# Kernel optimization log

Hardware: AMD Instinct MI355X
Metric: run time of the kernel (lower is better)

## Reference

```python
import jax, jax.numpy as jnp
import numpy as np

EPS = 1e-8  # RMSNormMultiHead default eps (forward passes self.eps)


def rms_norm_multihead(x, weight):
    # x: (B, L, H, d); normalize over last dim in float32, then scale per (H, d)
    x32 = x.astype(jnp.float32)
    normed = x32 * jax.lax.rsqrt(jnp.mean(x32 * x32, axis=-1, keepdims=True) + EPS)
    return normed.astype(x.dtype) * weight


def setup_inputs() -> dict:
    key = jax.random.key(0)
    k0, k1, k2 = jax.random.split(key, 3)
    B, L, D, H = 2, 1024, 1024, 16
    d = D // H
    X = jax.random.normal(k0, (B, L, D), dtype=jnp.float32)
    Wq = jax.random.normal(k1, (D, D), dtype=jnp.float32) * 0.02  # q_proj weight (out, in)
    Wv = jax.random.normal(k2, (D, D), dtype=jnp.float32) * 0.02  # v_proj weight (out, in)
    q_norm_w = jnp.ones((H, d), dtype=jnp.float32)
    v_norm_w = jnp.ones((H, d), dtype=jnp.float32)
    return {"X": X, "Wq": Wq, "Wv": Wv, "q_norm_w": q_norm_w, "v_norm_w": v_norm_w}


def reference(X, Wq, Wv, q_norm_w, v_norm_w):
    B, L, D = X.shape
    H, d = q_norm_w.shape
    K = X.reshape(B, L, H, d)
    Q = rms_norm_multihead((X @ Wq.T).reshape(B, L, H, d), q_norm_w)
    V = rms_norm_multihead((X @ Wv.T).reshape(B, L, H, d), v_norm_w)
    # cumulative outer-product KV state: (B, L, H, d, e)
    W = jnp.cumsum(jnp.einsum('blhd,blhe->blhde', K, V), axis=1)
    out = jnp.einsum('blhd,blhde->blhe', Q, W).reshape(B, L, D)
    return out
```

## Files before the change

kernel.cpp:

```cpp
#include <hip/hip_runtime.h>

#define BB 2
#define LL 1024
#define DD 1024
#define HH 16
#define NC 16
#define EPSF 1e-8f

typedef __attribute__((ext_vector_type(8))) short bf16x8;
typedef __attribute__((ext_vector_type(4))) float f32x4;
typedef unsigned short u16;

static __device__ inline u16 f2bf(float f) {
    unsigned int u = __builtin_bit_cast(unsigned int, f);
    u += 0x7fff + ((u >> 16) & 1);
    return (u16)(u >> 16);
}
static __device__ inline float bf2f(u16 v) {
    unsigned int u = ((unsigned int)v) << 16;
    return __builtin_bit_cast(float, u);
}
static __device__ inline void gload_lds16(const u16* g, u16* l) {
    __builtin_amdgcn_global_load_lds((const __attribute__((address_space(1))) void*)g,
                                     (__attribute__((address_space(3))) void*)l, 16, 0, 0);
}

__global__ __launch_bounds__(256) void cvt_k(const float* __restrict__ X,
                                             const float* __restrict__ Wq,
                                             const float* __restrict__ Wv,
                                             u16* __restrict__ Xb,
                                             u16* __restrict__ Wqb,
                                             u16* __restrict__ Wvb)
{
    int i = (blockIdx.x * 256 + threadIdx.x) * 4;
    const float* s; u16* d; int off;
    if (i < 2*1024*1024)      { s = X;  d = Xb;  off = i; }
    else if (i < 3*1024*1024) { s = Wq; d = Wqb; off = i - 2*1024*1024; }
    else                      { s = Wv; d = Wvb; off = i - 3*1024*1024; }
    float4 v = *(const float4*)(s + off);
    ushort4 o;
    o.x = f2bf(v.x); o.y = f2bf(v.y); o.z = f2bf(v.z); o.w = f2bf(v.w);
    *(ushort4*)(d + off) = o;
}

__global__ __launch_bounds__(256) void gemm_fused(const u16* __restrict__ Xb,
                                                  const u16* __restrict__ Wqb,
                                                  const u16* __restrict__ Wvb,
                                                  const float* __restrict__ qw,
                                                  const float* __restrict__ vw,
                                                  u16* __restrict__ Qb,
                                                  u16* __restrict__ Vb,
                                                  u16* __restrict__ S)
{
    const int K = DD, N = DD;
    const u16* W = blockIdx.z ? Wvb : Wqb;
    const float* nw = blockIdx.z ? vw : qw;
    u16* Y = blockIdx.z ? Vb : Qb;

    __shared__ alignas(16) char smem[49152];
    u16* Ab = (u16*)smem;
    u16* Bb = (u16*)(smem + 32768);

    const int tid = threadIdx.x, w = tid >> 6, lane = tid & 63;
    const int quad = lane >> 4, l16 = lane & 15;
    const int m0 = blockIdx.y * 128, n0 = blockIdx.x * 64;

    const int lr8 = lane >> 3;
    const int lc8 = (lane & 7) ^ lr8;
    const u16* gA = Xb + (size_t)(m0 + w*32 + lr8) * K + lc8 * 8;
    const u16* gB = W  + (size_t)(n0 + w*16 + lr8) * K + lc8 * 8;

    f32x4 acc[2][4] = {};

    auto stage = [&](int buf, int k0) {
        u16* As = Ab + buf * (128*64);
        u16* Bs = Bb + buf * (64*64);
        #pragma unroll
        for (int q = 0; q < 4; ++q)
            gload_lds16(gA + k0 + (size_t)q*8*K, As + (w*32 + q*8)*64);
        #pragma unroll
        for (int q = 0; q < 2; ++q)
            gload_lds16(gB + k0 + (size_t)q*8*K, Bs + (w*16 + q*8)*64);
    };
    auto compute = [&](int buf) {
        const u16* As = Ab + buf * (128*64);
        const u16* Bs = Bb + buf * (64*64);
        #pragma unroll
        for (int hh = 0; hh < 2; ++hh) {
            const int co = (((hh << 2) | quad) ^ (l16 & 7)) * 8;
            bf16x8 af[2], bfr[4];
            #pragma unroll
            for (int i = 0; i < 2; ++i)
                af[i] = *(const bf16x8*)&As[(w*32 + i*16 + l16) * 64 + co];
            #pragma unroll
            for (int j = 0; j < 4; ++j)
                bfr[j] = *(const bf16x8*)&Bs[(j*16 + l16) * 64 + co];
            #pragma unroll
            for (int i = 0; i < 2; ++i)
                #pragma unroll
                for (int j = 0; j < 4; ++j)
                    acc[i][j] = __builtin_amdgcn_mfma_f32_16x16x32_bf16(af[i], bfr[j], acc[i][j], 0, 0, 0);
        }
    };

    stage(0, 0);
    __syncthreads();
    int cur = 0;
    for (int k0 = 0; k0 < K; k0 += 64) {
        if (k0 + 64 < K) stage(cur ^ 1, k0 + 64);
        compute(cur);
        __syncthreads();
        cur ^= 1;
    }

    u16 (*Vt)[136] = (u16 (*)[136])smem;
    u16 (*Kt)[136] = (u16 (*)[136])(smem + 17408);

    float wv4[4];
    #pragma unroll
    for (int j = 0; j < 4; ++j) wv4[j] = nw[n0 + j*16 + l16];
    #pragma unroll
    for (int i = 0; i < 2; ++i) {
        float ss[4];
        #pragma unroll
        for (int r = 0; r < 4; ++r) {
            float s = 0.f;
            #pragma unroll
            for (int j = 0; j < 4; ++j) s += acc[i][j][r] * acc[i][j][r];
            ss[r] = s;
        }
        #pragma unroll
        for (int off = 1; off < 16; off <<= 1)
            #pragma unroll
            for (int r = 0; r < 4; ++r) ss[r] += __shfl_xor(ss[r], off, 64);
        float sc[4];
        #pragma unroll
        for (int r = 0; r < 4; ++r) sc[r] = rsqrtf(ss[r] * (1.f/64.f) + EPSF);
        #pragma unroll
        for (int r = 0; r < 4; ++r) {
            u16* yp = Y + (size_t)(m0 + w*32 + i*16 + quad*4 + r) * N + n0;
            #pragma unroll
            for (int j = 0; j < 4; ++j) {
                u16 val = f2bf(acc[i][j][r] * sc[r] * wv4[j]);
                yp[j*16 + l16] = val;
                if (blockIdx.z)
                    Vt[j*16 + l16][w*32 + i*16 + quad*4 + r] = val;
            }
        }
    }

    if (blockIdx.z) {
        {
            const int row = tid >> 1, q2 = tid & 1;
            size_t gb = (size_t)(m0 + row) * DD + n0 + q2 * 32;
            u16 kk[32];
            #pragma unroll
            for (int i2 = 0; i2 < 32; i2 += 4)
                *(ushort4*)&kk[i2] = *(const ushort4*)(Xb + gb + i2);
            #pragma unroll
            for (int i2 = 0; i2 < 32; ++i2)
                Kt[q2*32 + i2][row] = kk[i2];
        }
        __syncthreads();
        const int me = (w & 1) * 32, nd = (w >> 1) * 32;
        const int b = m0 >> 10, c0 = (m0 & 1023) >> 6, h = blockIdx.x;
        const int bh = b * HH + h;
        #pragma unroll
        for (int cc = 0; cc < 2; ++cc) {
            f32x4 sacc[2][2] = {};
            #pragma unroll
            for (int k0 = 0; k0 < 64; k0 += 32) {
                bf16x8 av[2], bv[2];
                #pragma unroll
                for (int i2 = 0; i2 < 2; ++i2)
                    av[i2] = *(const bf16x8*)&Vt[me + i2*16 + l16][cc*64 + k0 + quad*8];
                #pragma unroll
                for (int j2 = 0; j2 < 2; ++j2)
                    bv[j2] = *(const bf16x8*)&Kt[nd + j2*16 + l16][cc*64 + k0 + quad*8];
                #pragma unroll
                for (int i2 = 0; i2 < 2; ++i2)
                    #pragma unroll
                    for (int j2 = 0; j2 < 2; ++j2)
                        sacc[i2][j2] = __builtin_amdgcn_mfma_f32_16x16x32_bf16(av[i2], bv[j2], sacc[i2][j2], 0, 0, 0);
            }
            u16* Sp = S + ((size_t)((bh << 4) | (c0 + cc)) << 12) + w*1024;
            #pragma unroll
            for (int i2 = 0; i2 < 2; ++i2)
                #pragma unroll
                for (int j2 = 0; j2 < 2; ++j2)
                    #pragma unroll
                    for (int r = 0; r < 4; ++r)
                        Sp[(i2*2 + j2)*256 + r*64 + lane] = f2bf(sacc[i2][j2][r]);
        }
    }
}

__global__ __launch_bounds__(256) void out_k2(const u16* __restrict__ Xb,
                                              const u16* __restrict__ Qb,
                                              const u16* __restrict__ Vb,
                                              const u16* __restrict__ S,
                                              float* __restrict__ out)
{
    const int c = 15 - (blockIdx.x & 15);
    const int bh = blockIdx.x >> 4;
    const int h = bh & 15, b = bh >> 4;
    __shared__ u16 Qs[64][72];
    __shared__ u16 Ks[64][72];
    __shared__ u16 Vt[64][72];
    __shared__ u16 St[64][72];
    const int tid = threadIdx.x;
    {
        const int row = tid >> 2, q = tid & 3;
        size_t gbase = (size_t)(b*LL + c*64 + row) * DD + h*64 + q*16;
        u16 vv[16];
        #pragma unroll
        for (int i = 0; i < 16; i += 4) {
            *(ushort4*)&Qs[row][q*16 + i] = *(const ushort4*)(Qb + gbase + i);
            *(ushort4*)&Ks[row][q*16 + i] = *(const ushort4*)(Xb + gbase + i);
            *(ushort4*)&vv[i] = *(const ushort4*)(Vb + gbase + i);
        }
        #pragma unroll
        for (int i = 0; i < 16; ++i)
            Vt[q*16 + i][row] = vv[i];
        float facc[16] = {};
        const u16* Sbase = S + ((size_t)(bh * NC) << 12);
        int cp = 0;
        for (; cp + 4 <= c; cp += 4) {
            ushort4 sv[4][4];
            #pragma unroll
            for (int u = 0; u < 4; ++u)
                #pragma unroll
                for (int jj = 0; jj < 4; ++jj)
                    sv[u][jj] = *(const ushort4*)(Sbase + ((size_t)(cp + u) << 12) + tid*4 + jj*1024);
            #pragma unroll
            for (int u = 0; u < 4; ++u)
                #pragma unroll
                for (int jj = 0; jj < 4; ++jj) {
                    facc[jj*4+0] += bf2f(sv[u][jj].x);
                    facc[jj*4+1] += bf2f(sv[u][jj].y);
                    facc[jj*4+2] += bf2f(sv[u][jj].z);
                    facc[jj*4+3] += bf2f(sv[u][jj].w);
                }
        }
        for (; cp < c; ++cp) {
            const u16* Sc = Sbase + ((size_t)cp << 12);
            #pragma unroll
            for (int jj = 0; jj < 4; ++jj) {
                ushort4 sv = *(const ushort4*)(Sc + tid*4 + jj*1024);
                facc[jj*4+0] += bf2f(sv.x);
                facc[jj*4+1] += bf2f(sv.y);
                facc[jj*4+2] += bf2f(sv.z);
                facc[jj*4+3] += bf2f(sv.w);
            }
        }
        #pragma unroll
        for (int jj = 0; jj < 4; ++jj) {
            int g = tid * 4;
            int ij = (g >> 8) & 3, r = (g >> 6) & 3, ln = g & 63;
            int e = (jj & 1)*32 + (ij >> 1)*16 + (ln >> 4)*4 + r;
            int d = (jj >> 1)*32 + (ij & 1)*16 + (ln & 15);
            ushort4 o;
            o.x = f2bf(facc[jj*4+0]);
            o.y = f2bf(facc[jj*4+1]);
            o.z = f2bf(facc[jj*4+2]);
            o.w = f2bf(facc[jj*4+3]);
            *(ushort4*)&St[e][d] = o;
        }
    }
    __syncthreads();
    const int w = tid >> 6, lane = tid & 63, quad = lane >> 4, l16 = lane & 15;
    const int mo = (w & 1) * 32, no = (w >> 1) * 32;

    f32x4 pacc[2][2] = {};
    #pragma unroll
    for (int k0 = 0; k0 < 64; k0 += 32) {
        bf16x8 aq[2], bk[2];
        #pragma unroll
        for (int i = 0; i < 2; ++i)
            aq[i] = *(const bf16x8*)&Qs[mo + i*16 + l16][k0 + quad*8];
        #pragma unroll
        for (int j = 0; j < 2; ++j)
            bk[j] = *(const bf16x8*)&Ks[no + j*16 + l16][k0 + quad*8];
        #pragma unroll
        for (int i = 0; i < 2; ++i)
            #pragma unroll
            for (int j = 0; j < 2; ++j)
                pacc[i][j] = __builtin_amdgcn_mfma_f32_16x16x32_bf16(aq[i], bk[j], pacc[i][j], 0, 0, 0);
    }
    __syncthreads();
    #pragma unroll
    for (int i = 0; i < 2; ++i)
        #pragma unroll
        for (int j = 0; j < 2; ++j)
            #pragma unroll
            for (int r = 0; r < 4; ++r) {
                int l  = mo + i*16 + quad*4 + r;
                int lp = no + j*16 + l16;
                Ks[l][lp] = (lp <= l) ? f2bf(pacc[i][j][r]) : (u16)0;
            }
    __syncthreads();

    f32x4 acc[2][2] = {};
    #pragma unroll
    for (int k0 = 0; k0 < 64; k0 += 32) {
        bf16x8 a1[2], b1[2], a2[2], b2[2];
        #pragma unroll
        for (int i = 0; i < 2; ++i) {
            a1[i] = *(const bf16x8*)&Ks[mo + i*16 + l16][k0 + quad*8];
            a2[i] = *(const bf16x8*)&Qs[mo + i*16 + l16][k0 + quad*8];
        }
        #pragma unroll
        for (int j = 0; j < 2; ++j) {
            b1[j] = *(const bf16x8*)&Vt[no + j*16 + l16][k0 + quad*8];
            b2[j] = *(const bf16x8*)&St[no + j*16 + l16][k0 + quad*8];
        }
        #pragma unroll
        for (int i = 0; i < 2; ++i)
            #pragma unroll
            for (int j = 0; j < 2; ++j) {
                acc[i][j] = __builtin_amdgcn_mfma_f32_16x16x32_bf16(a1[i], b1[j], acc[i][j], 0, 0, 0);
                acc[i][j] = __builtin_amdgcn_mfma_f32_16x16x32_bf16(a2[i], b2[j], acc[i][j], 0, 0, 0);
            }
    }
    float* op = out + (size_t)(b*LL + c*64) * DD + h*64;
    #pragma unroll
    for (int i = 0; i < 2; ++i)
        #pragma unroll
        for (int j = 0; j < 2; ++j)
            #pragma unroll
            for (int r = 0; r < 4; ++r)
                op[(size_t)(mo + i*16 + quad*4 + r) * DD + no + j*16 + l16] = acc[i][j][r];
}

extern "C" void kernel_launch(void* const* d_in, const int* in_sizes, int n_in,
                              void* d_out, int out_size, void* d_ws, size_t ws_size,
                              hipStream_t stream) {
    const float* X  = (const float*)d_in[0];
    const float* Wq = (const float*)d_in[1];
    const float* Wv = (const float*)d_in[2];
    const float* qw = (const float*)d_in[3];
    const float* vw = (const float*)d_in[4];
    float* out = (float*)d_out;

    u16* Xb  = (u16*)d_ws;
    u16* Wqb = Xb  + (size_t)2*1024*1024;
    u16* Wvb = Wqb + (size_t)1024*1024;
    u16* Qb  = Wvb + (size_t)1024*1024;
    u16* Vb  = Qb  + (size_t)2*1024*1024;
    u16* S   = Vb  + (size_t)2*1024*1024;

    cvt_k<<<4096, 256, 0, stream>>>(X, Wq, Wv, Xb, Wqb, Wvb);
    gemm_fused<<<dim3(16, 16, 2), 256, 0, stream>>>(Xb, Wqb, Wvb, qw, vw, Qb, Vb, S);
    out_k2<<<BB*HH*NC, 256, 0, stream>>>(Xb, Qb, Vb, S, out);
}
```

Before: 96.96 us.

## Merge three kernels into one cooperative kernel with grid-wide syncs

Replaces the convert, GEMM+norm+chunk-state, and output kernels with a single persistent cooperative kernel of 512 blocks that uses grid syncs between phases. The aim is to remove the launch overhead and inter-kernel gaps of three separate dispatches. In exchange, every phase is fixed at 512 blocks, so the convert phase loops 8 times per thread. Grid barriers add their own latency, and the launch bound of 2 blocks per CU may constrain registers.

Measured after the change: 331.6 us. +242.0%, slower.

```diff
diff --git a/kernel.cpp b/kernel.cpp
--- a/kernel.cpp
+++ b/kernel.cpp
@@ -1,4 +1,6 @@
 #include <hip/hip_runtime.h>
+#include <hip/hip_cooperative_groups.h>
+namespace cg = cooperative_groups;
 
 #define BB 2
 #define LL 1024
@@ -25,311 +27,310 @@
                                      (__attribute__((address_space(3))) void*)l, 16, 0, 0);
 }
 
-__global__ __launch_bounds__(256) void cvt_k(const float* __restrict__ X,
-                                             const float* __restrict__ Wq,
-                                             const float* __restrict__ Wv,
-                                             u16* __restrict__ Xb,
-                                             u16* __restrict__ Wqb,
-                                             u16* __restrict__ Wvb)
+__global__ __launch_bounds__(256, 2) void fused_all(
+    const float* __restrict__ X, const float* __restrict__ Wq, const float* __restrict__ Wv,
+    const float* __restrict__ qw, const float* __restrict__ vw,
+    u16* __restrict__ Xb, u16* __restrict__ Wqb, u16* __restrict__ Wvb,
+    u16* __restrict__ Qb, u16* __restrict__ Vb, u16* __restrict__ S,
+    float* __restrict__ out)
 {
-    int i = (blockIdx.x * 256 + threadIdx.x) * 4;
-    const float* s; u16* d; int off;
-    if (i < 2*1024*1024)      { s = X;  d = Xb;  off = i; }
-    else if (i < 3*1024*1024) { s = Wq; d = Wqb; off = i - 2*1024*1024; }
-    else                      { s = Wv; d = Wvb; off = i - 3*1024*1024; }
-    float4 v = *(const float4*)(s + off);
-    ushort4 o;
-    o.x = f2bf(v.x); o.y = f2bf(v.y); o.z = f2bf(v.z); o.w = f2bf(v.w);
-    *(ushort4*)(d + off) = o;
-}
-
-__global__ __launch_bounds__(256) void gemm_fused(const u16* __restrict__ Xb,
-                                                  const u16* __restrict__ Wqb,
-                                                  const u16* __restrict__ Wvb,
-                                                  const float* __restrict__ qw,
-                                                  const float* __restrict__ vw,
-                                                  u16* __restrict__ Qb,
-                                                  u16* __restrict__ Vb,
-                                                  u16* __restrict__ S)
-{
-    const int K = DD, N = DD;
-    const u16* W = blockIdx.z ? Wvb : Wqb;
-    const float* nw = blockIdx.z ? vw : qw;
-    u16* Y = blockIdx.z ? Vb : Qb;
-
     __shared__ alignas(16) char smem[49152];
-    u16* Ab = (u16*)smem;
-    u16* Bb = (u16*)(smem + 32768);
-
-    const int tid = threadIdx.x, w = tid >> 6, lane = tid & 63;
+    const int tid = threadIdx.x;
+    const int bid = blockIdx.x;
+    const int w = tid >> 6, lane = tid & 63;
     const int quad = lane >> 4, l16 = lane & 15;
-    const int m0 = blockIdx.y * 128, n0 = blockIdx.x * 64;
-
-    const int lr8 = lane >> 3;
-    const int lc8 = (lane & 7) ^ lr8;
-    const u16* gA = Xb + (size_t)(m0 + w*32 + lr8) * K + lc8 * 8;
-    const u16* gB = W  + (size_t)(n0 + w*16 + lr8) * K + lc8 * 8;
-
-    f32x4 acc[2][4] = {};
-
-    auto stage = [&](int buf, int k0) {
-        u16* As = Ab + buf * (128*64);
-        u16* Bs = Bb + buf * (64*64);
-        #pragma unroll
-        for (int q = 0; q < 4; ++q)
-            gload_lds16(gA + k0 + (size_t)q*8*K, As + (w*32 + q*8)*64);
-        #pragma unroll
-        for (int q = 0; q < 2; ++q)
-            gload_lds16(gB + k0 + (size_t)q*8*K, Bs + (w*16 + q*8)*64);
-    };
-    auto compute = [&](int buf) {
-        const u16* As = Ab + buf * (128*64);
-        const u16* Bs = Bb + buf * (64*64);
-        #pragma unroll
-        for (int hh = 0; hh < 2; ++hh) {
-            const int co = (((hh << 2) | quad) ^ (l16 & 7)) * 8;
-            bf16x8 af[2], bfr[4];
-            #pragma unroll
-            for (int i = 0; i < 2; ++i)
-                af[i] = *(const bf16x8*)&As[(w*32 + i*16 + l16) * 64 + co];
-            #pragma unroll
-            for (int j = 0; j < 4; ++j)
-                bfr[j] = *(const bf16x8*)&Bs[(j*16 + l16) * 64 + co];
-            #pragma unroll
-            for (int i = 0; i < 2; ++i)
+
+    {
+        const int base = (bid * 256 + tid) * 4;
+        #pragma unroll
+        for (int it = 0; it < 8; ++it) {
+            int i = base + it * (512 * 256 * 4);
+            const float* s; u16* d; int off;
+            if (i < 2*1024*1024)      { s = X;  d = Xb;  off = i; }
+            else if (i < 3*1024*1024) { s = Wq; d = Wqb; off = i - 2*1024*1024; }
+            else                      { s = Wv; d = Wvb; off = i - 3*1024*1024; }
+            float4 v = *(const float4*)(s + off);
+            ushort4 o;
+            o.x = f2bf(v.x); o.y = f2bf(v.y); o.z = f2bf(v.z); o.w = f2bf(v.w);
+            *(ushort4*)(d + off) = o;
+        }
+    }
+    __threadfence();
+    cg::this_grid().sync();
+
+    {
+        const int K = DD, N = DD;
+        const int z = bid >> 8;
+        const int m0 = ((bid >> 4) & 15) * 128, n0 = (bid & 15) * 64;
+        const u16* W = z ? Wvb : Wqb;
+        const float* nw = z ? vw : qw;
+        u16* Y = z ? Vb : Qb;
+
+        u16* Ab = (u16*)smem;
+        u16* Bb = (u16*)(smem + 32768);
+
+        const int lr8 = lane >> 3;
+        const int lc8 = (lane & 7) ^ lr8;
+        const u16* gA = Xb + (size_t)(m0 + w*32 + lr8) * K + lc8 * 8;
+        const u16* gB = W  + (size_t)(n0 + w*16 + lr8) * K + lc8 * 8;
+
+        f32x4 acc[2][4] = {};
+
+        auto stage = [&](int buf, int k0) {
+            u16* As = Ab + buf * (128*64);
+            u16* Bs = Bb + buf * (64*64);
+            #pragma unroll
+            for (int q = 0; q < 4; ++q)
+                gload_lds16(gA + k0 + (size_t)q*8*K, As + (w*32 + q*8)*64);
+            #pragma unroll
+            for (int q = 0; q < 2; ++q)
+                gload_lds16(gB + k0 + (size_t)q*8*K, Bs + (w*16 + q*8)*64);
+        };
+        auto compute = [&](int buf) {
+            const u16* As = Ab + buf * (128*64);
+            const u16* Bs = Bb + buf * (64*64);
+            #pragma unroll
+            for (int hh = 0; hh < 2; ++hh) {
+                const int co = (((hh << 2) | quad) ^ (l16 & 7)) * 8;
+                bf16x8 af[2], bfr[4];
+                #pragma unroll
+                for (int i = 0; i < 2; ++i)
+                    af[i] = *(const bf16x8*)&As[(w*32 + i*16 + l16) * 64 + co];
                 #pragma unroll
                 for (int j = 0; j < 4; ++j)
-                    acc[i][j] = __builtin_amdgcn_mfma_f32_16x16x32_bf16(af[i], bfr[j], acc[i][j], 0, 0, 0);
-        }
-    };
-
-    stage(0, 0);
-    __syncthreads();
-    int cur = 0;
-    for (int k0 = 0; k0 < K; k0 += 64) {
-        if (k0 + 64 < K) stage(cur ^ 1, k0 + 64);
-        compute(cur);
+                    bfr[j] = *(const bf16x8*)&Bs[(j*16 + l16) * 64 + co];
+                #pragma unroll
+                for (int i = 0; i < 2; ++i)
+                    #pragma unroll
+                    for (int j = 0; j < 4; ++j)
+                        acc[i][j] = __builtin_amdgcn_mfma_f32_16x16x32_bf16(af[i], bfr[j], acc[i][j], 0, 0, 0);
+            }
+        };
+
+        stage(0, 0);
         __syncthreads();
-        cur ^= 1;
-    }
-
-    u16 (*Vt)[136] = (u16 (*)[136])smem;
-    u16 (*Kt)[136] = (u16 (*)[136])(smem + 17408);
-
-    float wv4[4];
-    #pragma unroll
-    for (int j = 0; j < 4; ++j) wv4[j] = nw[n0 + j*16 + l16];
-    #pragma unroll
-    for (int i = 0; i < 2; ++i) {
-        float ss[4];
-        #pragma unroll
-        for (int r = 0; r < 4; ++r) {
-            float s = 0.f;
-            #pragma unroll
-            for (int j = 0; j < 4; ++j) s += acc[i][j][r] * acc[i][j][r];
-            ss[r] = s;
-        }
-        #pragma unroll
-        for (int off = 1; off < 16; off <<= 1)
-            #pragma unroll
-            for (int r = 0; r < 4; ++r) ss[r] += __shfl_xor(ss[r], off, 64);
-        float sc[4];
-        #pragma unroll
-        for (int r = 0; r < 4; ++r) sc[r] = rsqrtf(ss[r] * (1.f/64.f) + EPSF);
-        #pragma unroll
-        for (int r = 0; r < 4; ++r) {
-            u16* yp = Y + (size_t)(m0 + w*32 + i*16 + quad*4 + r) * N + n0;
-            #pragma unroll
-            for (int j = 0; j < 4; ++j) {
-                u16 val = f2bf(acc[i][j][r] * sc[r] * wv4[j]);
-                yp[j*16 + l16] = val;
-                if (blockIdx.z)
-                    Vt[j*16 + l16][w*32 + i*16 + quad*4 + r] = val;
-            }
-        }
-    }
-
-    if (blockIdx.z) {
-        {
-            const int row = tid >> 1, q2 = tid & 1;
-            size_t gb = (size_t)(m0 + row) * DD + n0 + q2 * 32;
-            u16 kk[32];
-            #pragma unroll
-            for (int i2 = 0; i2 < 32; i2 += 4)
-                *(ushort4*)&kk[i2] = *(const ushort4*)(Xb + gb + i2);
-            #pragma unroll
-            for (int i2 = 0; i2 < 32; ++i2)
-                Kt[q2*32 + i2][row] = kk[i2];
-        }
-        __syncthreads();
-        const int me = (w & 1) * 32, nd = (w >> 1) * 32;
-        const int b = m0 >> 10, c0 = (m0 & 1023) >> 6, h = blockIdx.x;
-        const int bh = b * HH + h;
-        #pragma unroll
-        for (int cc = 0; cc < 2; ++cc) {
-            f32x4 sacc[2][2] = {};
-            #pragma unroll
-            for (int k0 = 0; k0 < 64; k0 += 32) {
-                bf16x8 av[2], bv[2];
+        int cur = 0;
+        for (int k0 = 0; k0 < K; k0 += 64) {
+            if (k0 + 64 < K) stage(cur ^ 1, k0 + 64);
+            compute(cur);
+            __syncthreads();
+            cur ^= 1;
+        }
+
+        u16 (*Vt)[136] = (u16 (*)[136])smem;
+        u16 (*Kt)[136] = (u16 (*)[136])(smem + 17408);
+
+        float wv4[4];
+        #pragma unroll
+        for (int j = 0; j < 4; ++j) wv4[j] = nw[n0 + j*16 + l16];
+        #pragma unroll
+        for (int i = 0; i < 2; ++i) {
+            float ss[4];
+            #pragma unroll
+            for (int r = 0; r < 4; ++r) {
+                float s = 0.f;
+                #pragma unroll
+                for (int j = 0; j < 4; ++j) s += acc[i][j][r] * acc[i][j][r];
+                ss[r] = s;
+            }
+            #pragma unroll
+            for (int off = 1; off < 16; off <<= 1)
+                #pragma unroll
+                for (int r = 0; r < 4; ++r) ss[r] += __shfl_xor(ss[r], off, 64);
+            float sc[4];
+            #pragma unroll
+            for (int r = 0; r < 4; ++r) sc[r] = rsqrtf(ss[r] * (1.f/64.f) + EPSF);
+            #pragma unroll
+            for (int r = 0; r < 4; ++r) {
+                u16* yp = Y + (size_t)(m0 + w*32 + i*16 + quad*4 + r) * N + n0;
+                #pragma unroll
+                for (int j = 0; j < 4; ++j) {
+                    u16 val = f2bf(acc[i][j][r] * sc[r] * wv4[j]);
+                    yp[j*16 + l16] = val;
+                    if (z)
+                        Vt[j*16 + l16][w*32 + i*16 + quad*4 + r] = val;
+                }
+            }
+        }
+
+        if (z) {
+            {
+                const int row = tid >> 1, q2 = tid & 1;
+                size_t gb = (size_t)(m0 + row) * DD + n0 + q2 * 32;
+                u16 kk[32];
+                #pragma unroll
+                for (int i2 = 0; i2 < 32; i2 += 4)
+                    *(ushort4*)&kk[i2] = *(const ushort4*)(Xb + gb + i2);
+                #pragma unroll
+                for (int i2 = 0; i2 < 32; ++i2)
+                    Kt[q2*32 + i2][row] = kk[i2];
+            }
+            __syncthreads();
+            const int me = (w & 1) * 32, nd = (w >> 1) * 32;
+            const int bb_ = m0 >> 10, c0 = (m0 & 1023) >> 6, h = bid & 15;
+            const int bh = bb_ * HH + h;
+            #pragma unroll
+            for (int cc = 0; cc < 2; ++cc) {
+                f32x4 sacc[2][2] = {};
+                #pragma unroll
+                for (int k0 = 0; k0 < 64; k0 += 32) {
+                    bf16x8 av[2], bv[2];
+                    #pragma unroll
+                    for (int i2 = 0; i2 < 2; ++i2)
+                        av[i2] = *(const bf16x8*)&Vt[me + i2*16 + l16][cc*64 + k0 + quad*8];
+                    #pragma unroll
+                    for (int j2 = 0; j2 < 2; ++j2)
+                        bv[j2] = *(const bf16x8*)&Kt[nd + j2*16 + l16][cc*64 + k0 + quad*8];
+                    #pragma unroll
+                    for (int i2 = 0; i2 < 2; ++i2)
+                        #pragma unroll
+                        for (int j2 = 0; j2 < 2; ++j2)
+                            sacc[i2][j2] = __builtin_amdgcn_mfma_f32_16x16x32_bf16(av[i2], bv[j2], sacc[i2][j2], 0, 0, 0);
+                }
+                u16* Sp = S + ((size_t)((bh << 4) | (c0 + cc)) << 12) + w*1024;
                 #pragma unroll
                 for (int i2 = 0; i2 < 2; ++i2)
-                    av[i2] = *(const bf16x8*)&Vt[me + i2*16 + l16][cc*64 + k0 + quad*8];
-                #pragma unroll
-                for (int j2 = 0; j2 < 2; ++j2)
-                    bv[j2] = *(const bf16x8*)&Kt[nd + j2*16 + l16][cc*64 + k0 + quad*8];
-                #pragma unroll
-                for (int i2 = 0; i2 < 2; ++i2)
                     #pragma unroll
                     for (int j2 = 0; j2 < 2; ++j2)
-                        sacc[i2][j2] = __builtin_amdgcn_mfma_f32_16x16x32_bf16(av[i2], bv[j2], sacc[i2][j2], 0, 0, 0);
-            }
-            u16* Sp = S + ((size_t)((bh << 4) | (c0 + cc)) << 12) + w*1024;
-            #pragma unroll
-            for (int i2 = 0; i2 < 2; ++i2)
-                #pragma unroll
-                for (int j2 = 0; j2 < 2; ++j2)
-                    #pragma unroll
-                    for (int r = 0; r < 4; ++r)
-                        Sp[(i2*2 + j2)*256 + r*64 + lane] = f2bf(sacc[i2][j2][r]);
-        }
-    }
-}
-
-__global__ __launch_bounds__(256) void out_k2(const u16* __restrict__ Xb,
-                                              const u16* __restrict__ Qb,
-                                              const u16* __restrict__ Vb,
-                                              const u16* __restrict__ S,
-                                              float* __restrict__ out)
-{
-    const int c = 15 - (blockIdx.x & 15);
-    const int bh = blockIdx.x >> 4;
-    const int h = bh & 15, b = bh >> 4;
-    __shared__ u16 Qs[64][72];
-    __shared__ u16 Ks[64][72];
-    __shared__ u16 Vt[64][72];
-    __shared__ u16 St[64][72];
-    const int tid = threadIdx.x;
-    {
-        const int row = tid >> 2, q = tid & 3;
-        size_t gbase = (size_t)(b*LL + c*64 + row) * DD + h*64 + q*16;
-        u16 vv[16];
-        #pragma unroll
-        for (int i = 0; i < 16; i += 4) {
-            *(ushort4*)&Qs[row][q*16 + i] = *(const ushort4*)(Qb + gbase + i);
-            *(ushort4*)&Ks[row][q*16 + i] = *(const ushort4*)(Xb + gbase + i);
-            *(ushort4*)&vv[i] = *(const ushort4*)(Vb + gbase + i);
-        }
-        #pragma unroll
-        for (int i = 0; i < 16; ++i)
-            Vt[q*16 + i][row] = vv[i];
-        float facc[16] = {};
-        const u16* Sbase = S + ((size_t)(bh * NC) << 12);
-        int cp = 0;
-        for (; cp + 4 <= c; cp += 4) {
-            ushort4 sv[4][4];
-            #pragma unroll
-            for (int u = 0; u < 4; ++u)
-                #pragma unroll
-                for (int jj = 0; jj < 4; ++jj)
-                    sv[u][jj] = *(const ushort4*)(Sbase + ((size_t)(cp + u) << 12) + tid*4 + jj*1024);
-            #pragma unroll
-            for (int u = 0; u < 4; ++u)
-                #pragma unroll
-                for (int jj = 0; jj < 4; ++jj) {
-                    facc[jj*4+0] += bf2f(sv[u][jj].x);
-                    facc[jj*4+1] += bf2f(sv[u][jj].y);
-                    facc[jj*4+2] += bf2f(sv[u][jj].z);
-                    facc[jj*4+3] += bf2f(sv[u][jj].w);
-                }
-        }
-        for (; cp < c; ++cp) {
-            const u16* Sc = Sbase + ((size_t)cp << 12);
-            #pragma unroll
-            for (int jj = 0; jj < 4; ++jj) {
-                ushort4 sv = *(const ushort4*)(Sc + tid*4 + jj*1024);
-                facc[jj*4+0] += bf2f(sv.x);
-                facc[jj*4+1] += bf2f(sv.y);
-                facc[jj*4+2] += bf2f(sv.z);
-                facc[jj*4+3] += bf2f(sv.w);
-            }
-        }
-        #pragma unroll
-        for (int jj = 0; jj < 4; ++jj) {
-            int g = tid * 4;
-            int ij = (g >> 8) & 3, r = (g >> 6) & 3, ln = g & 63;
-            int e = (jj & 1)*32 + (ij >> 1)*16 + (ln >> 4)*4 + r;
-            int d = (jj >> 1)*32 + (ij & 1)*16 + (ln & 15);
-            ushort4 o;
-            o.x = f2bf(facc[jj*4+0]);
-            o.y = f2bf(facc[jj*4+1]);
-            o.z = f2bf(facc[jj*4+2]);
-            o.w = f2bf(facc[jj*4+3]);
-            *(ushort4*)&St[e][d] = o;
+                        #pragma unroll
+                        for (int r = 0; r < 4; ++r)
+                            Sp[(i2*2 + j2)*256 + r*64 + lane] = f2bf(sacc[i2][j2][r]);
+            }
         }
     }
     __syncthreads();
-    const int w = tid >> 6, lane = tid & 63, quad = lane >> 4, l16 = lane & 15;
-    const int mo = (w & 1) * 32, no = (w >> 1) * 32;
-
-    f32x4 pacc[2][2] = {};
-    #pragma unroll
-    for (int k0 = 0; k0 < 64; k0 += 32) {
-        bf16x8 aq[2], bk[2];
+    __threadfence();
+    cg::this_grid().sync();
+
+    {
+        const int c = 15 - (bid & 15);
+        const int bh = bid >> 4;
+        const int h = bh & 15, b = bh >> 4;
+        u16 (*Qs)[72] = (u16 (*)[72])smem;
+        u16 (*Ks)[72] = (u16 (*)[72])(smem + 9216);
+        u16 (*Vt)[72] = (u16 (*)[72])(smem + 18432);
+        u16 (*St)[72] = (u16 (*)[72])(smem + 27648);
+        {
+            const int row = tid >> 2, q = tid & 3;
+            size_t gbase = (size_t)(b*LL + c*64 + row) * DD + h*64 + q*16;
+            u16 vv[16];
+            #pragma unroll
+            for (int i = 0; i < 16; i += 4) {
+                *(ushort4*)&Qs[row][q*16 + i] = *(const ushort4*)(Qb + gbase + i);
+                *(ushort4*)&Ks[row][q*16 + i] = *(const ushort4*)(Xb + gbase + i);
+                *(ushort4*)&vv[i] = *(const ushort4*)(Vb + gbase + i);
+            }
+            #pragma unroll
+            for (int i = 0; i < 16; ++i)
+                Vt[q*16 + i][row] = vv[i];
+            float facc[16] = {};
+            const u16* Sbase = S + ((size_t)(bh * NC) << 12);
+            int cp = 0;
+            for (; cp + 4 <= c; cp += 4) {
+                ushort4 sv[4][4];
+                #pragma unroll
+                for (int u = 0; u < 4; ++u)
+                    #pragma unroll
+                    for (int jj = 0; jj < 4; ++jj)
+                        sv[u][jj] = *(const ushort4*)(Sbase + ((size_t)(cp + u) << 12) + tid*4 + jj*1024);
+                #pragma unroll
+                for (int u = 0; u < 4; ++u)
+                    #pragma unroll
+                    for (int jj = 0; jj < 4; ++jj) {
+                        facc[jj*4+0] += bf2f(sv[u][jj].x);
+                        facc[jj*4+1] += bf2f(sv[u][jj].y);
+                        facc[jj*4+2] += bf2f(sv[u][jj].z);
+                        facc[jj*4+3] += bf2f(sv[u][jj].w);
+                    }
+            }
+            for (; cp < c; ++cp) {
+                const u16* Sc = Sbase + ((size_t)cp << 12);
+                #pragma unroll
+                for (int jj = 0; jj < 4; ++jj) {
+                    ushort4 sv = *(const ushort4*)(Sc + tid*4 + jj*1024);
+                    facc[jj*4+0] += bf2f(sv.x);
+                    facc[jj*4+1] += bf2f(sv.y);
+                    facc[jj*4+2] += bf2f(sv.z);
+                    facc[jj*4+3] += bf2f(sv.w);
+                }
+            }
+            #pragma unroll
+            for (int jj = 0; jj < 4; ++jj) {
+                int g = tid * 4;
+                int ij = (g >> 8) & 3, r = (g >> 6) & 3, ln = g & 63;
+                int e = (jj & 1)*32 + (ij >> 1)*16 + (ln >> 4)*4 + r;
+                int d = (jj >> 1)*32 + (ij & 1)*16 + (ln & 15);
+                ushort4 o;
+                o.x = f2bf(facc[jj*4+0]);
+                o.y = f2bf(facc[jj*4+1]);
+                o.z = f2bf(facc[jj*4+2]);
+                o.w = f2bf(facc[jj*4+3]);
+                *(ushort4*)&St[e][d] = o;
+            }
+        }
+        __syncthreads();
+        const int mo = (w & 1) * 32, no = (w >> 1) * 32;
+
+        f32x4 pacc[2][2] = {};
+        #pragma unroll
+        for (int k0 = 0; k0 < 64; k0 += 32) {
+            bf16x8 aq[2], bk[2];
+            #pragma unroll
+            for (int i = 0; i < 2; ++i)
+                aq[i] = *(const bf16x8*)&Qs[mo + i*16 + l16][k0 + quad*8];
+            #pragma unroll
+            for (int j = 0; j < 2; ++j)
+                bk[j] = *(const bf16x8*)&Ks[no + j*16 + l16][k0 + quad*8];
+            #pragma unroll
+            for (int i = 0; i < 2; ++i)
+                #pragma unroll
+                for (int j = 0; j < 2; ++j)
+                    pacc[i][j] = __builtin_amdgcn_mfma_f32_16x16x32_bf16(aq[i], bk[j], pacc[i][j], 0, 0, 0);
+        }
+        __syncthreads();
         #pragma unroll
         for (int i = 0; i < 2; ++i)
-            aq[i] = *(const bf16x8*)&Qs[mo + i*16 + l16][k0 + quad*8];
-        #pragma unroll
-        for (int j = 0; j < 2; ++j)
-            bk[j] = *(const bf16x8*)&Ks[no + j*16 + l16][k0 + quad*8];
+            #pragma unroll
+            for (int j = 0; j < 2; ++j)
+                #pragma unroll
+                for (int r = 0; r < 4; ++r) {
+                    int l  = mo + i*16 + quad*4 + r;
+                    int lp = no + j*16 + l16;
+                    Ks[l][lp] = (lp <= l) ? f2bf(pacc[i][j][r]) : (u16)0;
+                }
+        __syncthreads();
+
+        f32x4 acc[2][2] = {};
+        #pragma unroll
+        for (int k0 = 0; k0 < 64; k0 += 32) {
+            bf16x8 a1[2], b1[2], a2[2], b2[2];
+            #pragma unroll
+            for (int i = 0; i < 2; ++i) {
+                a1[i] = *(const bf16x8*)&Ks[mo + i*16 + l16][k0 + quad*8];
+                a2[i] = *(const bf16x8*)&Qs[mo + i*16 + l16][k0 + quad*8];
+            }
+            #pragma unroll
+            for (int j = 0; j < 2; ++j) {
+                b1[j] = *(const bf16x8*)&Vt[no + j*16 + l16][k0 + quad*8];
+                b2[j] = *(const bf16x8*)&St[no + j*16 + l16][k0 + quad*8];
+            }
+            #pragma unroll
+            for (int i = 0; i < 2; ++i)
+                #pragma unroll
+                for (int j = 0; j < 2; ++j) {
+                    acc[i][j] = __builtin_amdgcn_mfma_f32_16x16x32_bf16(a1[i], b1[j], acc[i][j], 0, 0, 0);
+                    acc[i][j] = __builtin_amdgcn_mfma_f32_16x16x32_bf16(a2[i], b2[j], acc[i][j], 0, 0, 0);
+                }
+        }
+        float* op = out + (size_t)(b*LL + c*64) * DD + h*64;
         #pragma unroll
         for (int i = 0; i < 2; ++i)
             #pragma unroll
             for (int j = 0; j < 2; ++j)
-                pacc[i][j] = __builtin_amdgcn_mfma_f32_16x16x32_bf16(aq[i], bk[j], pacc[i][j], 0, 0, 0);
+                #pragma unroll
+                for (int r = 0; r < 4; ++r)
+                    op[(size_t)(mo + i*16 + quad*4 + r) * DD + no + j*16 + l16] = acc[i][j][r];
     }
-    __syncthreads();
-    #pragma unroll
-    for (int i = 0; i < 2; ++i)
-        #pragma unroll
-        for (int j = 0; j < 2; ++j)
-            #pragma unroll
-            for (int r = 0; r < 4; ++r) {
-                int l  = mo + i*16 + quad*4 + r;
-                int lp = no + j*16 + l16;
-                Ks[l][lp] = (lp <= l) ? f2bf(pacc[i][j][r]) : (u16)0;
-            }
-    __syncthreads();
-
-    f32x4 acc[2][2] = {};
-    #pragma unroll
-    for (int k0 = 0; k0 < 64; k0 += 32) {
-        bf16x8 a1[2], b1[2], a2[2], b2[2];
-        #pragma unroll
-        for (int i = 0; i < 2; ++i) {
-            a1[i] = *(const bf16x8*)&Ks[mo + i*16 + l16][k0 + quad*8];
-            a2[i] = *(const bf16x8*)&Qs[mo + i*16 + l16][k0 + quad*8];
-        }
-        #pragma unroll
-        for (int j = 0; j < 2; ++j) {
-            b1[j] = *(const bf16x8*)&Vt[no + j*16 + l16][k0 + quad*8];
-            b2[j] = *(const bf16x8*)&St[no + j*16 + l16][k0 + quad*8];
-        }
-        #pragma unroll
-        for (int i = 0; i < 2; ++i)
-            #pragma unroll
-            for (int j = 0; j < 2; ++j) {
-                acc[i][j] = __builtin_amdgcn_mfma_f32_16x16x32_bf16(a1[i], b1[j], acc[i][j], 0, 0, 0);
-                acc[i][j] = __builtin_amdgcn_mfma_f32_16x16x32_bf16(a2[i], b2[j], acc[i][j], 0, 0, 0);
-            }
-    }
-    float* op = out + (size_t)(b*LL + c*64) * DD + h*64;
-    #pragma unroll
-    for (int i = 0; i < 2; ++i)
-        #pragma unroll
-        for (int j = 0; j < 2; ++j)
-            #pragma unroll
-            for (int r = 0; r < 4; ++r)
-                op[(size_t)(mo + i*16 + quad*4 + r) * DD + no + j*16 + l16] = acc[i][j][r];
 }
 
 extern "C" void kernel_launch(void* const* d_in, const int* in_sizes, int n_in,
@@ -349,7 +350,11 @@
     u16* Vb  = Qb  + (size_t)2*1024*1024;
     u16* S   = Vb  + (size_t)2*1024*1024;
 
-    cvt_k<<<4096, 256, 0, stream>>>(X, Wq, Wv, Xb, Wqb, Wvb);
-    gemm_fused<<<dim3(16, 16, 2), 256, 0, stream>>>(Xb, Wqb, Wvb, qw, vw, Qb, Vb, S);
-    out_k2<<<BB*HH*NC, 256, 0, stream>>>(Xb, Qb, Vb, S, out);
-}
+    void* args[12];
+    args[0]  = (void*)&X;   args[1]  = (void*)&Wq;  args[2]  = (void*)&Wv;
+    args[3]  = (void*)&qw;  args[4]  = (void*)&vw;
+    args[5]  = (void*)&Xb;  args[6]  = (void*)&Wqb; args[7]  = (void*)&Wvb;
+    args[8]  = (void*)&Qb;  args[9]  = (void*)&Vb;  args[10] = (void*)&S;
+    args[11] = (void*)&out;
+    hipLaunchCooperativeKernel((const void*)fused_all, dim3(512), dim3(256), args, 0, stream);
+}
```
